# Optimization experiments

Hardware: AMD Instinct MI355X
Metric: run time of the kernel (lower is better)

The kernel has to match this reference:

```python
import jax, jax.numpy as jnp
import numpy as np

B, C, P, T, H = 4, 256, 1024, 64, 8
D = C // H
SCALE = float(np.sqrt(D * T))


def setup_inputs() -> dict:
    key = jax.random.key(0)
    ks = jax.random.split(key, 7)
    s = 1.0 / np.sqrt(C)
    return {
        "x": jax.random.normal(ks[0], (B, C, P, T), dtype=jnp.float32),
        "Wk": jax.random.uniform(ks[1], (C, C), dtype=jnp.float32, minval=-s, maxval=s),
        "bk": jax.random.uniform(ks[2], (C,), dtype=jnp.float32, minval=-s, maxval=s),
        "Wq": jax.random.uniform(ks[3], (C, C), dtype=jnp.float32, minval=-s, maxval=s),
        "bq": jax.random.uniform(ks[4], (C,), dtype=jnp.float32, minval=-s, maxval=s),
        "Wv": jax.random.uniform(ks[5], (C, C), dtype=jnp.float32, minval=-s, maxval=s),
        "bv": jax.random.uniform(ks[6], (C,), dtype=jnp.float32, minval=-s, maxval=s),
    }


def _proj_split(x, W, b):
    # 1x1 conv == channel-mixing linear; then split heads: b (h d) p t -> b h d p t
    y = jnp.einsum('bcpt,oc->bopt', x, W) + b[None, :, None, None]
    Bs, _, Ps, Ts = y.shape
    return y.reshape(Bs, H, D, Ps, Ts)


def reference(x, Wk, bk, Wq, bq, Wv, bv):
    k = _proj_split(x, Wk, bk)
    q = _proj_split(x, Wq, bq)
    v = _proj_split(x, Wv, bv)
    # contract jointly over d and t
    energy = jnp.einsum('bhdpt,bhdqt->bhpq', k, q)
    attn = jax.nn.softmax(energy / SCALE, axis=-1)
    out = jnp.einsum('bhpq,bhdpt->bhdqt', attn, v)
    # merge heads: b h d q t -> b (h d) q t
    return out.reshape(B, C, P, T)
```

## Files before the change

kernel.cpp:

```cpp
#include <hip/hip_runtime.h>
#include <cstdint>
#include <cstddef>

#define NB 4
#define NC 256
#define NP 1024
#define NT 64
#define NH 8
#define ND 32
#define NF 2048
#define NPT 65536
#define KQV_ELEMS 67108864ull
#define INV_SCALE 0.022097086912079608f

typedef unsigned short u16;
typedef __bf16 bf16x8 __attribute__((ext_vector_type(8)));
typedef short  s16x8  __attribute__((ext_vector_type(8)));
typedef short  s16x4  __attribute__((ext_vector_type(4)));
typedef float  f32x4  __attribute__((ext_vector_type(4)));

__device__ __forceinline__ u16 f2bf(float f) {
  unsigned u = __builtin_bit_cast(unsigned, f);
  u += 0x7fffu + ((u >> 16) & 1u);
  return (u16)(u >> 16);
}
__device__ __forceinline__ float bf2f(u16 h) {
  unsigned u = ((unsigned)h) << 16;
  return __builtin_bit_cast(float, u);
}
__device__ __forceinline__ int swz(int row) { return ((row ^ (row >> 3)) & 7) << 4; }

#define GLOAD_LDS16(gp, lp) __builtin_amdgcn_global_load_lds( \
    (const __attribute__((address_space(1))) void*)(gp),      \
    (__attribute__((address_space(3))) void*)(lp), 16, 0, 0)

__device__ __forceinline__ f32x4 mfma16(bf16x8 a, bf16x8 b, f32x4 c) {
  return __builtin_amdgcn_mfma_f32_16x16x32_bf16(a, b, c, 0, 0, 0);
}

__global__ __launch_bounds__(256) void wcast_kernel(
    const float* __restrict__ Wk, const float* __restrict__ Wq,
    const float* __restrict__ Wv, u16* __restrict__ wbf)
{
  int pj = blockIdx.y;
  const float* W = (pj == 0) ? Wk : ((pj == 1) ? Wq : Wv);
  int idx = blockIdx.x * 1024 + threadIdx.x * 4;
  float4 v = *(const float4*)(W + idx);
  s16x4 pk;
  pk[0] = (short)f2bf(v.x); pk[1] = (short)f2bf(v.y);
  pk[2] = (short)f2bf(v.z); pk[3] = (short)f2bf(v.w);
  *(s16x4*)(wbf + (size_t)pj * 65536 + idx) = pk;
}

__global__ __launch_bounds__(256, 2) void xcast_kernel(
    const float* __restrict__ x, u16* __restrict__ xT)
{
  int ptt = blockIdx.x;
  int ct  = blockIdx.y;
  int b   = blockIdx.z;
  __shared__ __align__(16) u16 L[64 * 64];
  int tid = threadIdx.x;
#pragma unroll
  for (int i = 0; i < 4; i++) {
    int cl  = i * 16 + (tid >> 4);
    int ptl = (tid & 15) * 4;
    float4 v = *(const float4*)(x + ((size_t)(b * NC + ct * 64 + cl)) * NPT +
                                ptt * 64 + ptl);
    s16x4 pk;
    pk[0] = (short)f2bf(v.x); pk[1] = (short)f2bf(v.y);
    pk[2] = (short)f2bf(v.z); pk[3] = (short)f2bf(v.w);
    *(s16x4*)((char*)L + ((cl * 128 + ptl * 2) ^ swz(cl))) = pk;
  }
  __syncthreads();
#pragma unroll
  for (int i = 0; i < 2; i++) {
    int ptl = i * 32 + (tid >> 3);
    int c8  = (tid & 7) * 8;
    s16x8 v;
#pragma unroll
    for (int j = 0; j < 8; j++) {
      int row = c8 + j;
      v[j] = (short)*(const u16*)((char*)L + ((row * 128 + ptl * 2) ^ swz(row)));
    }
    *(s16x8*)(xT + ((size_t)b * NPT + (size_t)ptt * 64 + ptl) * NC + ct * 64 + c8) = v;
  }
}

__global__ __launch_bounds__(256, 2) void transpose_kernel(
    const u16* __restrict__ in, u16* __restrict__ outp)
{
  int ft = blockIdx.x;
  int pt = blockIdx.y;
  int slab = blockIdx.z;
  __shared__ __align__(16) u16 L[64 * 64];
  int t = threadIdx.x;
  const u16* ip = in + (size_t)slab * NP * NF;
#pragma unroll
  for (int i = 0; i < 2; i++) {
    int pl = i * 32 + (t >> 3);
    int c8 = (t & 7) * 8;
    s16x8 v = *(const s16x8*)(ip + (size_t)(pt * 64 + pl) * NF + ft * 64 + c8);
    *(s16x8*)((char*)L + ((pl * 128 + c8 * 2) ^ swz(pl))) = v;
  }
  __syncthreads();
  u16* op = outp + (size_t)slab * NP * NF;
#pragma unroll
  for (int i = 0; i < 2; i++) {
    int fl = i * 32 + (t >> 3);
    int p8 = (t & 7) * 8;
    s16x8 v;
#pragma unroll
    for (int j2 = 0; j2 < 8; j2++) {
      int row = p8 + j2;
      v[j2] = (short)*(const u16*)((char*)L + ((row * 128 + fl * 2) ^ swz(row)));
    }
    *(s16x8*)(op + (size_t)(ft * 64 + fl) * NP + pt * 64 + p8) = v;
  }
}

#define STG1(TT, I, OP) do {                                                   \
    const u16* gp_ = (OP ? Bg : Ag) + (size_t)grow[I] * KT + (TT) * 32 + gcol[I]; \
    GLOAD_LDS16(gp_, L + ((((TT) & 3) * 32768 + (OP) * 16384 +                 \
                           ((I) & 1 ? W1 : W0)) >> 1));                        \
  } while (0)

#define FENCE() do {                                                           \
    asm volatile("" ::: "memory");                                             \
    __builtin_amdgcn_sched_barrier(0);                                         \
  } while (0)

#define KBODY(J, WAITASM, DOSTG) do {                                          \
    const int bufb_ = ((J) & 3) * 32768;                                       \
    bf16x8 a_[4], b_[4];                                                       \
    _Pragma("unroll")                                                          \
    for (int mf = 0; mf < 4; mf++)                                             \
      a_[mf] = *(const bf16x8*)((const char*)L + bufb_ + baseA + mf * 1024);   \
    _Pragma("unroll")                                                          \
    for (int nf = 0; nf < 4; nf++)                                             \
      b_[nf] = *(const bf16x8*)((const char*)L + bufb_ + baseB + nf * 1024);   \
    if (DOSTG) { STG1((J) + 3, 0, 0); STG1((J) + 3, 1, 0); }                   \
    __builtin_amdgcn_s_barrier();                                              \
    asm volatile("s_waitcnt lgkmcnt(0)" ::: "memory");                         \
    __builtin_amdgcn_sched_barrier(0);                                         \
    __builtin_amdgcn_s_setprio(1);                                             \
    _Pragma("unroll")                                                          \
    for (int mf = 0; mf < 4; mf++)                                             \
      _Pragma("unroll")                                                        \
      for (int nf = 0; nf < 4; nf++)                                           \
        acc[mf][nf] = mfma16(a_[mf], b_[nf], acc[mf][nf]);                     \
    __builtin_amdgcn_s_setprio(0);                                             \
    __builtin_amdgcn_sched_barrier(0);                                         \
    __builtin_amdgcn_s_barrier();                                              \
    FENCE();                                                                   \
    bf16x8 a2_[4];                                                             \
    _Pragma("unroll")                                                          \
    for (int mf = 0; mf < 4; mf++)                                             \
      a2_[mf] = *(const bf16x8*)((const char*)L + bufb_ + baseA +              \
                                 (4 + mf) * 1024);                             \
    if (DOSTG) { STG1((J) + 3, 2, 1); STG1((J) + 3, 3, 1); }                   \
    __builtin_amdgcn_s_barrier();                                              \
    asm volatile("s_waitcnt lgkmcnt(0)" ::: "memory");                         \
    __builtin_amdgcn_sched_barrier(0);                                         \
    __builtin_amdgcn_s_setprio(1);                                             \
    _Pragma("unroll")                                                          \
    for (int mf = 0; mf < 4; mf++)                                             \
      _Pragma("unroll")                                                        \
      for (int nf = 0; nf < 4; nf++)                                           \
        acc[4 + mf][nf] = mfma16(a2_[mf], b_[nf], acc[4 + mf][nf]);            \
    __builtin_amdgcn_s_setprio(0);                                             \
    __builtin_amdgcn_sched_barrier(0);                                         \
    asm volatile(WAITASM ::: "memory");                                        \
    __builtin_amdgcn_s_barrier();                                              \
    FENCE();                                                                   \
  } while (0)

template <int KT>
__device__ __forceinline__ void core256(const u16* __restrict__ Ag,
                                        const u16* __restrict__ Bg,
                                        u16* L, f32x4 acc[8][4])
{
  constexpr int NKT = KT / 32;
  const int tid  = threadIdx.x;
  const int lane = tid & 63;
  const int wv   = tid >> 6;
  const int wr = wv >> 2, wc = wv & 3;

  int grow[4], gcol[4];
#pragma unroll
  for (int i = 0; i < 4; i++) {
    int oi   = (tid + (i & 1) * 512) * 16;
    int loff = oi ^ (((oi >> 6) & 3) << 4);
    grow[i] = loff >> 6;
    gcol[i] = (loff & 63) >> 1;
  }
  const int W0 = wv * 1024;
  const int W1 = wv * 1024 + 8192;

  const int rowA  = wr * 128 + (lane & 15);
  const int baseA = rowA * 64 + (((lane >> 4) * 16) ^ ((rowA & 3) << 4));
  const int rowB  = wc * 64 + (lane & 15);
  const int baseB = 16384 + rowB * 64 + (((lane >> 4) * 16) ^ ((rowB & 3) << 4));

#pragma unroll
  for (int tt = 0; tt < 3; tt++) {
    STG1(tt, 0, 0); STG1(tt, 1, 0); STG1(tt, 2, 1); STG1(tt, 3, 1);
  }
  __builtin_amdgcn_sched_barrier(0);
  asm volatile("s_waitcnt vmcnt(8)" ::: "memory");
  __builtin_amdgcn_s_barrier();
  FENCE();

  for (int j = 0; j < NKT - 3; ++j)
    KBODY(j, "s_waitcnt vmcnt(8)", 1);
  KBODY(NKT - 3, "s_waitcnt vmcnt(4)", 0);
  KBODY(NKT - 2, "s_waitcnt vmcnt(0)", 0);
  KBODY(NKT - 1, "", 0);
}

__global__ __launch_bounds__(512, 1) void proj256_kernel(
    const u16* __restrict__ wbf, const u16* __restrict__ xT,
    const float* __restrict__ bk, const float* __restrict__ bq,
    const float* __restrict__ bv, u16* __restrict__ kqv)
{
  extern __shared__ u16 L[];
  int d0 = blockIdx.x;
  int b  = blockIdx.y;
  int xcd = d0 & 7, r = d0 >> 3;
  int pj  = r % 3, tch = r / 3;
  int ptile = tch * 8 + xcd;
  const float* bias = (pj == 0) ? bk : ((pj == 1) ? bq : bv);
  u16* outb = kqv + (size_t)pj * KQV_ELEMS;
  const int n0 = ptile * 256;

  const u16* Ag = wbf + (size_t)pj * 65536;
  const u16* Bg = xT + ((size_t)b * NPT + (size_t)n0) * NC;

  f32x4 acc[8][4];
#pragma unroll
  for (int a = 0; a < 8; a++)
#pragma unroll
    for (int c = 0; c < 4; c++) acc[a][c] = (f32x4){0.f, 0.f, 0.f, 0.f};

  core256<NC>(Ag, Bg, L, acc);

  const int lane = threadIdx.x & 63, wv = threadIdx.x >> 6;
  const int wr = wv >> 2, wc = wv & 3;
#pragma unroll
  for (int mf = 0; mf < 8; mf++) {
#pragma unroll
    for (int jj = 0; jj < 4; jj++) {
      int o = wr * 128 + mf * 16 + (lane >> 4) * 4 + jj;
      float bsv = bias[o];
      int hh = o >> 5, dd = o & 31;
#pragma unroll
      for (int nf = 0; nf < 4; nf++) {
        int n = n0 + wc * 64 + nf * 16 + (lane & 15);
        int p = n >> 6, t = n & 63;
        outb[((size_t)(b * NH + hh) * NP + p) * NF + dd * 64 + t] =
            f2bf(acc[mf][nf][jj] + bsv);
      }
    }
  }
}

__global__ __launch_bounds__(512, 2) void qk256_kernel(
    const u16* __restrict__ kb, const u16* __restrict__ qb, u16* __restrict__ S)
{
  extern __shared__ u16 L[];
  int bid = blockIdx.x;
  int xcd = bid & 7, r = bid >> 3;
  int bh  = xcd * 4 + (r >> 4);
  int til = r & 15;
  int mt  = til >> 2, nt = til & 3;

  const u16* Ag = qb + (size_t)bh * NP * NF + (size_t)mt * 256 * NF;
  const u16* Bg = kb + (size_t)bh * NP * NF + (size_t)nt * 256 * NF;

  f32x4 acc[8][4];
#pragma unroll
  for (int a = 0; a < 8; a++)
#pragma unroll
    for (int c = 0; c < 4; c++) acc[a][c] = (f32x4){0.f, 0.f, 0.f, 0.f};

  core256<NF>(Ag, Bg, L, acc);

  const int lane = threadIdx.x & 63, wv = threadIdx.x >> 6;
  const int wr = wv >> 2, wc = wv & 3;
  u16* Sp = S + (size_t)bh * NP * NP;
#pragma unroll
  for (int mf = 0; mf < 8; mf++)
#pragma unroll
    for (int jj = 0; jj < 4; jj++) {
      int m = mt * 256 + wr * 128 + mf * 16 + (lane >> 4) * 4 + jj;
#pragma unroll
      for (int nf = 0; nf < 4; nf++) {
        int n = nt * 256 + wc * 64 + nf * 16 + (lane & 15);
        Sp[(size_t)m * NP + n] = f2bf(acc[mf][nf][jj] * INV_SCALE);
      }
    }
}

__global__ __launch_bounds__(512, 2) void av256_kernel(
    const u16* __restrict__ Ab, const u16* __restrict__ Vt, float* __restrict__ out)
{
  extern __shared__ u16 L[];
  int bid = blockIdx.x;
  int xcd = bid & 7, r = bid >> 3;
  int bh  = xcd * 4 + (r >> 5);
  int til = r & 31;
  int mt  = til >> 3, ntf = til & 7;

  const u16* Ag = Ab + (size_t)bh * NP * NP + (size_t)mt * 256 * NP;
  const u16* Bg = Vt + (size_t)bh * NF * NP + (size_t)ntf * 256 * NP;

  f32x4 acc[8][4];
#pragma unroll
  for (int a = 0; a < 8; a++)
#pragma unroll
    for (int c = 0; c < 4; c++) acc[a][c] = (f32x4){0.f, 0.f, 0.f, 0.f};

  core256<NP>(Ag, Bg, L, acc);

  const int lane = threadIdx.x & 63, wv = threadIdx.x >> 6;
  const int wr = wv >> 2, wc = wv & 3;
  int b = bh >> 3, h = bh & 7;
#pragma unroll
  for (int mf = 0; mf < 8; mf++)
#pragma unroll
    for (int jj = 0; jj < 4; jj++) {
      int m = mt * 256 + wr * 128 + mf * 16 + (lane >> 4) * 4 + jj;
#pragma unroll
      for (int nf = 0; nf < 4; nf++) {
        int n = ntf * 256 + wc * 64 + nf * 16 + (lane & 15);
        int dd = n >> 6, t = n & 63;
        out[((size_t)(b * NC + h * ND + dd) * NP + m) * NT + t] = acc[mf][nf][jj];
      }
    }
}

__global__ __launch_bounds__(256, 2) void softmax_kernel(
    const u16* __restrict__ S, u16* __restrict__ A)
{
  int cb = blockIdx.x;
  int bh = blockIdx.y;
  int tid = threadIdx.x;
  int cg  = tid & 7;
  int qs  = tid >> 3;
  int col0 = cb * 64 + cg * 8;
  const u16* Sp = S + (size_t)bh * NP * NP + col0;

  float m[8], l[8];
#pragma unroll
  for (int j2 = 0; j2 < 8; j2++) { m[j2] = -1e30f; l[j2] = 0.f; }
  for (int q = qs * 32; q < qs * 32 + 32; q++) {
    s16x8 v = *(const s16x8*)(Sp + (size_t)q * NP);
#pragma unroll
    for (int j2 = 0; j2 < 8; j2++) {
      float f = bf2f((u16)v[j2]);
      float mn = fmaxf(m[j2], f);
      l[j2] = l[j2] * __expf(m[j2] - mn) + __expf(f - mn);
      m[j2] = mn;
    }
  }
  __shared__ float ms[32][64], ls[32][64];
#pragma unroll
  for (int j2 = 0; j2 < 8; j2++) {
    ms[qs][cg * 8 + j2] = m[j2];
    ls[qs][cg * 8 + j2] = l[j2];
  }
  __syncthreads();
  float M[8], Li[8];
#pragma unroll
  for (int j2 = 0; j2 < 8; j2++) {
    int c = cg * 8 + j2;
    float mm = ms[0][c];
#pragma unroll
    for (int k = 1; k < 32; k++) mm = fmaxf(mm, ms[k][c]);
    float ll = 0.f;
#pragma unroll
    for (int k = 0; k < 32; k++) ll += ls[k][c] * __expf(ms[k][c] - mm);
    M[j2] = mm; Li[j2] = 1.f / ll;
  }
  u16* Ap = A + (size_t)bh * NP * NP + col0;
  for (int q = qs * 32; q < qs * 32 + 32; q++) {
    s16x8 v = *(const s16x8*)(Sp + (size_t)q * NP);
    s16x8 o;
#pragma unroll
    for (int j2 = 0; j2 < 8; j2++)
      o[j2] = (short)f2bf(__expf(bf2f((u16)v[j2]) - M[j2]) * Li[j2]);
    *(s16x8*)(Ap + (size_t)q * NP) = o;
  }
}

extern "C" void kernel_launch(void* const* d_in, const int* in_sizes, int n_in,
                              void* d_out, int out_size, void* d_ws, size_t ws_size,
                              hipStream_t stream)
{
  if (ws_size < 4ull * KQV_ELEMS * sizeof(u16)) return;

  const float* x  = (const float*)d_in[0];
  const float* Wk = (const float*)d_in[1];
  const float* bk = (const float*)d_in[2];
  const float* Wq = (const float*)d_in[3];
  const float* bq = (const float*)d_in[4];
  const float* Wv = (const float*)d_in[5];
  const float* bv = (const float*)d_in[6];

  u16* kb = (u16*)d_ws;
  u16* qb = kb + KQV_ELEMS;
  u16* vb = kb + 2 * KQV_ELEMS;
  u16* vt = kb + 3 * KQV_ELEMS;

  u16* xT  = (u16*)d_out;
  u16* wbf = xT + KQV_ELEMS;
  u16* Sb  = xT + KQV_ELEMS + 262144;
  u16* Ab  = kb;

  (void)hipFuncSetAttribute((const void*)proj256_kernel,
                            hipFuncAttributeMaxDynamicSharedMemorySize, 131072);
  (void)hipFuncSetAttribute((const void*)qk256_kernel,
                            hipFuncAttributeMaxDynamicSharedMemorySize, 131072);
  (void)hipFuncSetAttribute((const void*)av256_kernel,
                            hipFuncAttributeMaxDynamicSharedMemorySize, 131072);

  wcast_kernel<<<dim3(64, 3), 256, 0, stream>>>(Wk, Wq, Wv, wbf);
  xcast_kernel<<<dim3(1024, 4, 4), 256, 0, stream>>>(x, xT);
  proj256_kernel<<<dim3(768, 4), 512, 131072, stream>>>(wbf, xT, bk, bq, bv, kb);
  transpose_kernel<<<dim3(32, 16, 32), 256, 0, stream>>>(vb, vt);
  qk256_kernel<<<dim3(512), 512, 131072, stream>>>(kb, qb, Sb);
  softmax_kernel<<<dim3(16, 32), 256, 0, stream>>>(Sb, Ab);
  av256_kernel<<<dim3(1024), 512, 131072, stream>>>(Ab, vt, (float*)d_out);
}
```

Measured before the change: 672.9 us.

## Replace projection GEMM with 1024-thread single-buffered kernel using static LDS

Swaps the 512-thread, 128 KB LDS, four-stage pipelined projection GEMM for a 1024-thread kernel. Each wave holds a 4x4 fragment tile, and the kernel uses a single 64 KB static LDS buffer with 64-wide K steps. Accumulators per wave drop from 32 to 16 fragments and LDS per block halves. The intent is to raise occupancy and latency hiding through more waves rather than software pipelining. In exchange it loses the overlap between global loads and MFMA, with barriers around each K step.

```diff
diff --git a/kernel.cpp b/kernel.cpp
--- a/kernel.cpp
+++ b/kernel.cpp
@@ -115,6 +115,98 @@
       v[j2] = (short)*(const u16*)((char*)L + ((row * 128 + fl * 2) ^ swz(row)));
     }
     *(s16x8*)(op + (size_t)(ft * 64 + fl) * NP + pt * 64 + p8) = v;
+  }
+}
+
+__global__ __launch_bounds__(1024) void proj1024_kernel(
+    const u16* __restrict__ wbf, const u16* __restrict__ xT,
+    const float* __restrict__ bk, const float* __restrict__ bq,
+    const float* __restrict__ bv, u16* __restrict__ kqv)
+{
+  __shared__ __align__(16) u16 L[32768];
+  int d0 = blockIdx.x;
+  int b  = blockIdx.y;
+  int xcd = d0 & 7, r = d0 >> 3;
+  int pj  = r % 3, tch = r / 3;
+  int ptile = tch * 8 + xcd;
+  const float* bias = (pj == 0) ? bk : ((pj == 1) ? bq : bv);
+  u16* outb = kqv + (size_t)pj * KQV_ELEMS;
+  const int n0 = ptile * 256;
+
+  const u16* Ag = wbf + (size_t)pj * 65536;
+  const u16* Bg = xT + ((size_t)b * NPT + (size_t)n0) * NC;
+
+  const int tid  = threadIdx.x;
+  const int lane = tid & 63;
+  const int wv   = tid >> 6;
+  const int wr = wv >> 2, wc = wv & 3;
+
+  int srow[2], scg;
+#pragma unroll
+  for (int i = 0; i < 2; i++) srow[i] = wv * 8 + i * 128 + (lane >> 3);
+  scg = (lane & 7) ^ ((lane >> 3) & 7);
+  const int dbase0 = wv * 1024;
+  const int dbase1 = wv * 1024 + 16384;
+
+  const int ra0 = wr * 64 + (lane & 15);
+  const int rb0 = wc * 64 + (lane & 15);
+
+  f32x4 acc[4][4];
+#pragma unroll
+  for (int a = 0; a < 4; a++)
+#pragma unroll
+    for (int c = 0; c < 4; c++) acc[a][c] = (f32x4){0.f, 0.f, 0.f, 0.f};
+
+  for (int ks = 0; ks < 4; ks++) {
+    const int k0 = ks * 64;
+    __syncthreads();
+#pragma unroll
+    for (int i = 0; i < 2; i++) {
+      GLOAD_LDS16(Ag + (size_t)srow[i] * NC + k0 + scg * 8,
+                  L + ((dbase0 + i * 16384) >> 1));
+      GLOAD_LDS16(Bg + (size_t)srow[i] * NC + k0 + scg * 8,
+                  L + ((32768 + dbase0 + i * 16384) >> 1));
+    }
+    __syncthreads();
+#pragma unroll
+    for (int kk = 0; kk < 2; kk++) {
+      bf16x8 af[4], bfr[4];
+#pragma unroll
+      for (int mf = 0; mf < 4; mf++) {
+        int ra = ra0 + mf * 16;
+        int g  = kk * 4 + (lane >> 4);
+        af[mf] = *(const bf16x8*)((char*)L + ra * 128 + ((g ^ (ra & 7)) << 4));
+      }
+#pragma unroll
+      for (int nf = 0; nf < 4; nf++) {
+        int rb = rb0 + nf * 16;
+        int g  = kk * 4 + (lane >> 4);
+        bfr[nf] = *(const bf16x8*)((char*)L + 32768 + rb * 128 +
+                                   ((g ^ (rb & 7)) << 4));
+      }
+#pragma unroll
+      for (int mf = 0; mf < 4; mf++)
+#pragma unroll
+        for (int nf = 0; nf < 4; nf++)
+          acc[mf][nf] = mfma16(af[mf], bfr[nf], acc[mf][nf]);
+    }
+  }
+
+#pragma unroll
+  for (int mf = 0; mf < 4; mf++) {
+#pragma unroll
+    for (int jj = 0; jj < 4; jj++) {
+      int o = wr * 64 + mf * 16 + (lane >> 4) * 4 + jj;
+      float bsv = bias[o];
+      int hh = o >> 5, dd = o & 31;
+#pragma unroll
+      for (int nf = 0; nf < 4; nf++) {
+        int n = n0 + wc * 64 + nf * 16 + (lane & 15);
+        int p = n >> 6, t = n & 63;
+        outb[((size_t)(b * NH + hh) * NP + p) * NF + dd * 64 + t] =
+            f2bf(acc[mf][nf][jj] + bsv);
+      }
+    }
   }
 }
 
@@ -217,52 +309,6 @@
   KBODY(NKT - 1, "", 0);
 }
 
-__global__ __launch_bounds__(512, 1) void proj256_kernel(
-    const u16* __restrict__ wbf, const u16* __restrict__ xT,
-    const float* __restrict__ bk, const float* __restrict__ bq,
-    const float* __restrict__ bv, u16* __restrict__ kqv)
-{
-  extern __shared__ u16 L[];
-  int d0 = blockIdx.x;
-  int b  = blockIdx.y;
-  int xcd = d0 & 7, r = d0 >> 3;
-  int pj  = r % 3, tch = r / 3;
-  int ptile = tch * 8 + xcd;
-  const float* bias = (pj == 0) ? bk : ((pj == 1) ? bq : bv);
-  u16* outb = kqv + (size_t)pj * KQV_ELEMS;
-  const int n0 = ptile * 256;
-
-  const u16* Ag = wbf + (size_t)pj * 65536;
-  const u16* Bg = xT + ((size_t)b * NPT + (size_t)n0) * NC;
-
-  f32x4 acc[8][4];
-#pragma unroll
-  for (int a = 0; a < 8; a++)
-#pragma unroll
-    for (int c = 0; c < 4; c++) acc[a][c] = (f32x4){0.f, 0.f, 0.f, 0.f};
-
-  core256<NC>(Ag, Bg, L, acc);
-
-  const int lane = threadIdx.x & 63, wv = threadIdx.x >> 6;
-  const int wr = wv >> 2, wc = wv & 3;
-#pragma unroll
-  for (int mf = 0; mf < 8; mf++) {
-#pragma unroll
-    for (int jj = 0; jj < 4; jj++) {
-      int o = wr * 128 + mf * 16 + (lane >> 4) * 4 + jj;
-      float bsv = bias[o];
-      int hh = o >> 5, dd = o & 31;
-#pragma unroll
-      for (int nf = 0; nf < 4; nf++) {
-        int n = n0 + wc * 64 + nf * 16 + (lane & 15);
-        int p = n >> 6, t = n & 63;
-        outb[((size_t)(b * NH + hh) * NP + p) * NF + dd * 64 + t] =
-            f2bf(acc[mf][nf][jj] + bsv);
-      }
-    }
-  }
-}
-
 __global__ __launch_bounds__(512, 2) void qk256_kernel(
     const u16* __restrict__ kb, const u16* __restrict__ qb, u16* __restrict__ S)
 {
@@ -416,8 +462,6 @@
   u16* Sb  = xT + KQV_ELEMS + 262144;
   u16* Ab  = kb;
 
-  (void)hipFuncSetAttribute((const void*)proj256_kernel,
-                            hipFuncAttributeMaxDynamicSharedMemorySize, 131072);
   (void)hipFuncSetAttribute((const void*)qk256_kernel,
                             hipFuncAttributeMaxDynamicSharedMemorySize, 131072);
   (void)hipFuncSetAttribute((const void*)av256_kernel,
@@ -425,7 +469,7 @@
 
   wcast_kernel<<<dim3(64, 3), 256, 0, stream>>>(Wk, Wq, Wv, wbf);
   xcast_kernel<<<dim3(1024, 4, 4), 256, 0, stream>>>(x, xT);
-  proj256_kernel<<<dim3(768, 4), 512, 131072, stream>>>(wbf, xT, bk, bq, bv, kb);
+  proj1024_kernel<<<dim3(768, 4), 1024, 0, stream>>>(wbf, xT, bk, bq, bv, kb);
   transpose_kernel<<<dim3(32, 16, 32), 256, 0, stream>>>(vb, vt);
   qk256_kernel<<<dim3(512), 512, 131072, stream>>>(kb, qb, Sb);
   softmax_kernel<<<dim3(16, 32), 256, 0, stream>>>(Sb, Ab);
```

Measured after the change: 681.5 us. Within noise of the previous version (+1.3%).

## Replace projection GEMM kernel with 1024-thread block using static 64KB LDS

Applied to the files above, without the earlier changes.

The projection GEMM moves from a 512-thread block with a 4-stage, 128KB dynamic-LDS pipeline to a 1024-thread block with a double-buffered 64KB static LDS tile and 4x4 MFMA fragments per wave. Each wave now holds half as many accumulators, and the smaller LDS footprint may let more blocks share a CU. The aim is better latency hiding through more waves instead of a deeper prefetch pipeline. In exchange, the prefetch depth drops to one tile and every k-step carries two block-wide barriers.

```diff
diff --git a/kernel.cpp b/kernel.cpp
--- a/kernel.cpp
+++ b/kernel.cpp
@@ -118,6 +118,112 @@
   }
 }
 
+#define PJSTG(TT) do {                                                         \
+    GLOAD_LDS16(Ag + (size_t)psrow * NC + (TT) * 32 + psg * 8,                 \
+                L + ((((TT) & 1) * 32768 + pdst) >> 1));                       \
+    GLOAD_LDS16(Bg + (size_t)psrow * NC + (TT) * 32 + psg * 8,                 \
+                L + ((((TT) & 1) * 32768 + 16384 + pdst) >> 1));               \
+  } while (0)
+
+#define PJBODY(J, WAITASM, DOSTG) do {                                         \
+    if (DOSTG) PJSTG((J) + 1);                                                 \
+    __builtin_amdgcn_sched_barrier(0);                                         \
+    asm volatile(WAITASM ::: "memory");                                        \
+    __builtin_amdgcn_s_barrier();                                              \
+    __builtin_amdgcn_sched_barrier(0);                                         \
+    {                                                                          \
+      const int bb = ((J) & 1) * 32768;                                        \
+      bf16x8 af[4], bfr[4];                                                    \
+      _Pragma("unroll")                                                        \
+      for (int mf = 0; mf < 4; mf++)                                           \
+        af[mf] = *(const bf16x8*)((char*)L + bb + baseA + mf * 1024);          \
+      _Pragma("unroll")                                                        \
+      for (int nf = 0; nf < 4; nf++)                                           \
+        bfr[nf] = *(const bf16x8*)((char*)L + bb + 16384 + baseB + nf * 1024); \
+      __builtin_amdgcn_s_setprio(1);                                           \
+      _Pragma("unroll")                                                        \
+      for (int mf = 0; mf < 4; mf++)                                           \
+        _Pragma("unroll")                                                      \
+        for (int nf = 0; nf < 4; nf++)                                         \
+          acc[mf][nf] = mfma16(af[mf], bfr[nf], acc[mf][nf]);                  \
+      __builtin_amdgcn_s_setprio(0);                                           \
+    }                                                                          \
+    __builtin_amdgcn_sched_barrier(0);                                         \
+    asm volatile("s_waitcnt lgkmcnt(0)" ::: "memory");                         \
+    __builtin_amdgcn_s_barrier();                                              \
+    asm volatile("" ::: "memory");                                             \
+    __builtin_amdgcn_sched_barrier(0);                                         \
+  } while (0)
+
+__global__ __launch_bounds__(1024) void proj1024_kernel(
+    const u16* __restrict__ wbf, const u16* __restrict__ xT,
+    const float* __restrict__ bk, const float* __restrict__ bq,
+    const float* __restrict__ bv, u16* __restrict__ kqv)
+{
+  __shared__ __align__(16) u16 L[32768];
+  int d0 = blockIdx.x;
+  int b  = blockIdx.y;
+  int xcd = d0 & 7, r = d0 >> 3;
+  int pj  = r % 3, tch = r / 3;
+  int ptile = tch * 8 + xcd;
+  const float* bias = (pj == 0) ? bk : ((pj == 1) ? bq : bv);
+  u16* outb = kqv + (size_t)pj * KQV_ELEMS;
+  const int n0 = ptile * 256;
+
+  const u16* Ag = wbf + (size_t)pj * 65536;
+  const u16* Bg = xT + ((size_t)b * NPT + (size_t)n0) * NC;
+
+  const int tid  = threadIdx.x;
+  const int lane = tid & 63;
+  const int wv   = tid >> 6;
+  const int wr = wv >> 2, wc = wv & 3;
+
+  const int psrow = tid >> 2;
+  const int psg   = (lane & 3) ^ ((lane >> 3) & 3);
+  const int pdst  = wv * 1024;
+
+  const int ra0 = wr * 64 + (lane & 15);
+  const int rb0 = wc * 64 + (lane & 15);
+  const int gk  = lane >> 4;
+  const int baseA = ra0 * 64 + ((gk ^ ((ra0 >> 1) & 3)) << 4);
+  const int baseB = rb0 * 64 + ((gk ^ ((rb0 >> 1) & 3)) << 4);
+
+  f32x4 acc[4][4];
+#pragma unroll
+  for (int a = 0; a < 4; a++)
+#pragma unroll
+    for (int c = 0; c < 4; c++) acc[a][c] = (f32x4){0.f, 0.f, 0.f, 0.f};
+
+  PJSTG(0);
+  __builtin_amdgcn_sched_barrier(0);
+
+  PJBODY(0, "s_waitcnt vmcnt(2)", 1);
+  PJBODY(1, "s_waitcnt vmcnt(2)", 1);
+  PJBODY(2, "s_waitcnt vmcnt(2)", 1);
+  PJBODY(3, "s_waitcnt vmcnt(2)", 1);
+  PJBODY(4, "s_waitcnt vmcnt(2)", 1);
+  PJBODY(5, "s_waitcnt vmcnt(2)", 1);
+  PJBODY(6, "s_waitcnt vmcnt(2)", 1);
+  PJBODY(7, "s_waitcnt vmcnt(0)", 0);
+
+#pragma unroll
+  for (int mf = 0; mf < 4; mf++) {
+#pragma unroll
+    for (int jj = 0; jj < 4; jj++) {
+      int o = wr * 64 + mf * 16 + (lane >> 4) * 4 + jj;
+      float bsv = bias[o];
+      int hh = o >> 5, dd = o & 31;
+#pragma unroll
+      for (int nf = 0; nf < 4; nf++) {
+        int n = n0 + wc * 64 + nf * 16 + (lane & 15);
+        int p = n >> 6, t = n & 63;
+        outb[((size_t)(b * NH + hh) * NP + p) * NF + dd * 64 + t] =
+            f2bf(acc[mf][nf][jj] + bsv);
+      }
+    }
+  }
+}
+
 #define STG1(TT, I, OP) do {                                                   \
     const u16* gp_ = (OP ? Bg : Ag) + (size_t)grow[I] * KT + (TT) * 32 + gcol[I]; \
     GLOAD_LDS16(gp_, L + ((((TT) & 3) * 32768 + (OP) * 16384 +                 \
@@ -217,52 +323,6 @@
   KBODY(NKT - 1, "", 0);
 }
 
-__global__ __launch_bounds__(512, 1) void proj256_kernel(
-    const u16* __restrict__ wbf, const u16* __restrict__ xT,
-    const float* __restrict__ bk, const float* __restrict__ bq,
-    const float* __restrict__ bv, u16* __restrict__ kqv)
-{
-  extern __shared__ u16 L[];
-  int d0 = blockIdx.x;
-  int b  = blockIdx.y;
-  int xcd = d0 & 7, r = d0 >> 3;
-  int pj  = r % 3, tch = r / 3;
-  int ptile = tch * 8 + xcd;
-  const float* bias = (pj == 0) ? bk : ((pj == 1) ? bq : bv);
-  u16* outb = kqv + (size_t)pj * KQV_ELEMS;
-  const int n0 = ptile * 256;
-
-  const u16* Ag = wbf + (size_t)pj * 65536;
-  const u16* Bg = xT + ((size_t)b * NPT + (size_t)n0) * NC;
-
-  f32x4 acc[8][4];
-#pragma unroll
-  for (int a = 0; a < 8; a++)
-#pragma unroll
-    for (int c = 0; c < 4; c++) acc[a][c] = (f32x4){0.f, 0.f, 0.f, 0.f};
-
-  core256<NC>(Ag, Bg, L, acc);
-
-  const int lane = threadIdx.x & 63, wv = threadIdx.x >> 6;
-  const int wr = wv >> 2, wc = wv & 3;
-#pragma unroll
-  for (int mf = 0; mf < 8; mf++) {
-#pragma unroll
-    for (int jj = 0; jj < 4; jj++) {
-      int o = wr * 128 + mf * 16 + (lane >> 4) * 4 + jj;
-      float bsv = bias[o];
-      int hh = o >> 5, dd = o & 31;
-#pragma unroll
-      for (int nf = 0; nf < 4; nf++) {
-        int n = n0 + wc * 64 + nf * 16 + (lane & 15);
-        int p = n >> 6, t = n & 63;
-        outb[((size_t)(b * NH + hh) * NP + p) * NF + dd * 64 + t] =
-            f2bf(acc[mf][nf][jj] + bsv);
-      }
-    }
-  }
-}
-
 __global__ __launch_bounds__(512, 2) void qk256_kernel(
     const u16* __restrict__ kb, const u16* __restrict__ qb, u16* __restrict__ S)
 {
@@ -416,8 +476,6 @@
   u16* Sb  = xT + KQV_ELEMS + 262144;
   u16* Ab  = kb;
 
-  (void)hipFuncSetAttribute((const void*)proj256_kernel,
-                            hipFuncAttributeMaxDynamicSharedMemorySize, 131072);
   (void)hipFuncSetAttribute((const void*)qk256_kernel,
                             hipFuncAttributeMaxDynamicSharedMemorySize, 131072);
   (void)hipFuncSetAttribute((const void*)av256_kernel,
@@ -425,7 +483,7 @@
 
   wcast_kernel<<<dim3(64, 3), 256, 0, stream>>>(Wk, Wq, Wv, wbf);
   xcast_kernel<<<dim3(1024, 4, 4), 256, 0, stream>>>(x, xT);
-  proj256_kernel<<<dim3(768, 4), 512, 131072, stream>>>(wbf, xT, bk, bq, bv, kb);
+  proj1024_kernel<<<dim3(768, 4), 1024, 0, stream>>>(wbf, xT, bk, bq, bv, kb);
   transpose_kernel<<<dim3(32, 16, 32), 256, 0, stream>>>(vb, vt);
   qk256_kernel<<<dim3(512), 512, 131072, stream>>>(kb, qb, Sb);
   softmax_kernel<<<dim3(16, 32), 256, 0, stream>>>(Sb, Ab);
```

New measurement: 675.1 us. Within noise of the previous version (+0.3%).
